# Performance work log

Hardware: AMD Instinct MI355X
Metric: run time of the kernel (lower is better)

The kernel has to match this reference:

```python
import jax, jax.numpy as jnp
import numpy as np

N_HEAD = 8
EPS = 1e-08


def setup_inputs() -> dict:
    key = jax.random.key(0)
    ks = jax.random.split(key, 4)
    B, T, C = 2, 2048, 512
    x = jax.random.normal(ks[0], (B, T, C), dtype=jnp.float32)
    attention_mask = jnp.ones((B, T, T), dtype=jnp.float32)  # causal structure irrelevant: only diagonal used
    c_attn_kernel = jax.random.normal(ks[1], (C, 3 * C), dtype=jnp.float32) * 0.02
    c_attn_bias = jnp.zeros((3 * C,), dtype=jnp.float32)
    c_proj_kernel = jax.random.normal(ks[2], (C, C), dtype=jnp.float32) * (0.02 / np.sqrt(2 * 12))
    c_proj_bias = jnp.zeros((C,), dtype=jnp.float32)
    return {
        "x": x,
        "attention_mask": attention_mask,
        "c_attn_kernel": c_attn_kernel,
        "c_attn_bias": c_attn_bias,
        "c_proj_kernel": c_proj_kernel,
        "c_proj_bias": c_proj_bias,
    }


def reference(x, attention_mask, c_attn_kernel, c_attn_bias, c_proj_kernel, c_proj_bias):
    B, T, C = x.shape
    H = N_HEAD
    D = C // H

    qkv = x @ c_attn_kernel + c_attn_bias            # (B,T,3C)
    q, k, v = jnp.split(qkv, 3, axis=2)

    # (B,T,C) -> (B,H,T,D)
    def to_heads(t):
        return t.reshape(B, T, H, D).transpose(0, 2, 1, 3)

    q, k, v = to_heads(q), to_heads(k), to_heads(v)

    phi_q = jax.nn.elu(q) + 1.0
    phi_k = jax.nn.elu(k) + 1.0

    valid_positions = jnp.diagonal(attention_mask, axis1=1, axis2=2)  # (B,T)
    position_mask = valid_positions[:, None, :, None]                 # (B,1,T,1)
    phi_k = phi_k * position_mask
    v = v * position_mask

    # (B,H,T,D,D) outer products, cumulative over time (memory-bound hot spot)
    kv_outer = jnp.einsum('bhti,bhtj->bhtij', phi_k, v)
    kv_cumsum = jnp.cumsum(kv_outer, axis=2)
    k_cumsum = jnp.cumsum(phi_k, axis=2)

    numerator = jnp.einsum('bhti,bhtij->bhtj', phi_q, kv_cumsum)      # (B,H,T,D)
    denominator = jnp.einsum('bhti,bhti->bht', phi_q, k_cumsum)       # (B,H,T)
    denominator = jnp.maximum(denominator, EPS)

    y = numerator / denominator[..., None]
    y = y.transpose(0, 2, 1, 3).reshape(B, T, C)
    y = y @ c_proj_kernel + c_proj_bias
    return y
```

## Files before the change

### kernel.cpp

```cpp
#include <hip/hip_runtime.h>
#include <math.h>

using short8 = __attribute__((ext_vector_type(8))) short;
using f32x4  = __attribute__((ext_vector_type(4))) float;
using us4    = __attribute__((ext_vector_type(4))) unsigned short;
typedef unsigned short ushort_t;

#define MFMA16(a,b,c) __builtin_amdgcn_mfma_f32_16x16x32_bf16((a),(b),(c),0,0,0)

#define BB 2
#define TT 2048
#define CC 512
#define HH 8
#define DD 64
#define N3 1536
#define NCH 32

__device__ __forceinline__ float bf2f(ushort_t u){ unsigned int x=((unsigned int)u)<<16; return __builtin_bit_cast(float,x); }
__device__ __forceinline__ ushort_t f2bf(float f){ unsigned int u=__builtin_bit_cast(unsigned int,f); u += 0x7FFFu + ((u>>16)&1u); return (ushort_t)(u>>16); }
__device__ __forceinline__ float elu1(float v){ return v > 0.f ? v + 1.f : expf(v); }

__global__ __launch_bounds__(256) void prep(const float* __restrict__ x, const float* __restrict__ amask,
                     const float* __restrict__ W, const float* __restrict__ Pw,
                     ushort_t* __restrict__ xb, ushort_t* __restrict__ wt,
                     ushort_t* __restrict__ pt, float* __restrict__ mdiag)
{
  __shared__ float tile[32][33];
  int bid = blockIdx.x, tid = threadIdx.x;
  int tx = tid & 31, ty0 = tid >> 5;
  if (bid < 768) {
    int nt = bid % 48, kt = bid / 48;
    #pragma unroll
    for (int i=0;i<4;++i){ int ty=ty0+8*i; tile[ty][tx] = W[(size_t)(kt*32+ty)*N3 + nt*32+tx]; }
    __syncthreads();
    #pragma unroll
    for (int i=0;i<4;++i){ int ty=ty0+8*i; wt[(size_t)(nt*32+ty)*CC + kt*32+tx] = f2bf(tile[tx][ty]); }
  } else if (bid < 1024) {
    int tt = bid - 768; int nt = tt & 15, kt = tt >> 4;
    #pragma unroll
    for (int i=0;i<4;++i){ int ty=ty0+8*i; tile[ty][tx] = Pw[(size_t)(kt*32+ty)*CC + nt*32+tx]; }
    __syncthreads();
    #pragma unroll
    for (int i=0;i<4;++i){ int ty=ty0+8*i; pt[(size_t)(nt*32+ty)*CC + kt*32+tx] = f2bf(tile[tx][ty]); }
  } else if (bid < 1056) {
    int g = (bid-1024)*256 + tid;
    const f32x4* xs = (const f32x4*)x;
    us4* xo = (us4*)xb;
    for (int i=g; i<(BB*TT*CC)/4; i+=32*256) {
      f32x4 v = xs[i];
      us4 o = { f2bf(v[0]), f2bf(v[1]), f2bf(v[2]), f2bf(v[3]) };
      xo[i] = o;
    }
  } else {
    for (int i=tid; i<BB*TT; i+=256) { int b=i>>11, t=i&2047; mdiag[i]=amask[((size_t)b*TT+t)*TT+t]; }
  }
}

__global__ __launch_bounds__(256) void gemm_qkv(const ushort_t* __restrict__ A, const ushort_t* __restrict__ Bt,
    const float* __restrict__ bias, const float* __restrict__ mdiag,
    ushort_t* __restrict__ phiQ, ushort_t* __restrict__ phiK,
    ushort_t* __restrict__ kTc, ushort_t* __restrict__ vTc)
{
  __shared__ __align__(16) ushort_t smem[128*72 + 64*72];
  ushort_t (*lA)[72] = (ushort_t(*)[72])smem;
  ushort_t (*lB)[72] = (ushort_t(*)[72])(smem + 128*72);
  const int tid = threadIdx.x;
  const int lane = tid & 63, wid = tid >> 6;
  const int g = lane >> 4, lr = lane & 15;
  const int bx = blockIdx.x, bm = blockIdx.y * 128;
  const int bn = bx * 64;
  const int wm = (wid >> 1) * 64, wn = (wid & 1) * 32;
  f32x4 acc[4][2] = {};

  {
    short8 nA[4], nB[2];
    #pragma unroll
    for (int it=0; it<4; ++it) { int fl = tid + it*256; nA[it] = *(const short8*)&A[(size_t)(bm + (fl>>3))*CC + (fl&7)*8]; }
    #pragma unroll
    for (int it=0; it<2; ++it) { int fl = tid + it*256; nB[it] = *(const short8*)&Bt[(size_t)(bn + (fl>>3))*CC + (fl&7)*8]; }
    #pragma unroll
    for (int it=0; it<4; ++it) { int fl = tid + it*256; *(short8*)&lA[fl>>3][(fl&7)*8] = nA[it]; }
    #pragma unroll
    for (int it=0; it<2; ++it) { int fl = tid + it*256; *(short8*)&lB[fl>>3][(fl&7)*8] = nB[it]; }
  }
  __syncthreads();

  #pragma unroll
  for (int t = 0; t < 8; ++t) {
    short8 nA[4], nB[2];
    if (t < 7) {
      int k0 = (t+1)*64;
      #pragma unroll
      for (int it=0; it<4; ++it) { int fl = tid + it*256; nA[it] = *(const short8*)&A[(size_t)(bm + (fl>>3))*CC + k0 + (fl&7)*8]; }
      #pragma unroll
      for (int it=0; it<2; ++it) { int fl = tid + it*256; nB[it] = *(const short8*)&Bt[(size_t)(bn + (fl>>3))*CC + k0 + (fl&7)*8]; }
    }
    short8 af[4][2], bf[2][2];
    #pragma unroll
    for (int mf=0; mf<4; ++mf)
      #pragma unroll
      for (int kk=0; kk<2; ++kk) af[mf][kk] = *(const short8*)&lA[wm + mf*16 + lr][kk*32 + g*8];
    #pragma unroll
    for (int nf=0; nf<2; ++nf)
      #pragma unroll
      for (int kk=0; kk<2; ++kk) bf[nf][kk] = *(const short8*)&lB[wn + nf*16 + lr][kk*32 + g*8];
    #pragma unroll
    for (int kk=0; kk<2; ++kk)
      #pragma unroll
      for (int mf=0; mf<4; ++mf)
        #pragma unroll
        for (int nf=0; nf<2; ++nf)
          acc[mf][nf] = MFMA16(af[mf][kk], bf[nf][kk], acc[mf][nf]);
    __syncthreads();
    if (t < 7) {
      #pragma unroll
      for (int it=0; it<4; ++it) { int fl = tid + it*256; *(short8*)&lA[fl>>3][(fl&7)*8] = nA[it]; }
      #pragma unroll
      for (int it=0; it<2; ++it) { int fl = tid + it*256; *(short8*)&lB[fl>>3][(fl&7)*8] = nB[it]; }
      __syncthreads();
    }
  }

  const int third = bx >> 3, h = bx & 7;
  const int b0 = bm >> 11;
  const size_t bh = (size_t)(b0*HH + h);
  ushort_t (*ldsT)[136] = (ushort_t(*)[136])smem;
  #pragma unroll
  for (int mf=0; mf<4; ++mf) {
    #pragma unroll
    for (int nf=0; nf<2; ++nf) {
      int d = wn + nf*16 + lr;
      float bs = bias[third*512 + h*64 + d];
      #pragma unroll
      for (int r=0; r<4; ++r) {
        int tl = wm + mf*16 + g*4 + r;
        int mm = bm + tl;
        int tg = mm & 2047;
        float v = acc[mf][nf][r] + bs;
        if (third == 0) {
          phiQ[(bh*TT + tg)*DD + d] = f2bf(elu1(v));
        } else if (third == 1) {
          ushort_t e = f2bf(elu1(v) * mdiag[mm]);
          phiK[(bh*TT + tg)*DD + d] = e;
          ldsT[d][tl] = e;
        } else {
          ldsT[d][tl] = f2bf(v * mdiag[mm]);
        }
      }
    }
  }
  if (third >= 1) {
    __syncthreads();
    ushort_t* dst = (third == 1) ? kTc : vTc;
    int d = tid >> 2, q = tid & 3;
    int cl = q >> 1, tl0 = (q & 1) * 32;
    int c0 = ((bm & 2047) >> 6) + cl;
    size_t obase = ((bh*NCH + c0)*DD + d)*64 + tl0;
    #pragma unroll
    for (int j=0; j<4; ++j)
      *(short8*)&dst[obase + j*8] = *(const short8*)&ldsT[d][cl*64 + tl0 + j*8];
  }
}

__global__ __launch_bounds__(256) void chunk_state(const ushort_t* __restrict__ kTc,
                                                   const ushort_t* __restrict__ vTc,
                                                   float* __restrict__ sChunk)
{
  int cid = blockIdx.x;
  int w = threadIdx.x >> 6;
  int lane = threadIdx.x & 63, g = lane >> 4, lr = lane & 15;
  size_t base = (size_t)cid * (DD*64);
  short8 af[4][2];
  #pragma unroll
  for (int mf=0; mf<4; ++mf)
    #pragma unroll
    for (int kf=0; kf<2; ++kf)
      af[mf][kf] = *(const short8*)&kTc[base + (size_t)(mf*16+lr)*64 + kf*32 + g*8];
  float* dst = &sChunk[(size_t)cid * 5120];
  short8 bfr[2];
  #pragma unroll
  for (int kf=0; kf<2; ++kf)
    bfr[kf] = *(const short8*)&vTc[base + (size_t)(w*16+lr)*64 + kf*32 + g*8];
  #pragma unroll
  for (int mf=0; mf<4; ++mf) {
    f32x4 acc = {0.f,0.f,0.f,0.f};
    #pragma unroll
    for (int kf=0; kf<2; ++kf) acc = MFMA16(af[mf][kf], bfr[kf], acc);
    *(f32x4*)&dst[(size_t)(w*16+lr)*64 + mf*16 + g*4] = acc;
  }
  if (w == 0) {
    short8 onesf;
    short ov = (lr == 0) ? (short)0x3F80 : (short)0;
    #pragma unroll
    for (int j=0;j<8;++j) onesf[j] = ov;
    #pragma unroll
    for (int mf=0; mf<4; ++mf) {
      f32x4 acc = {0.f,0.f,0.f,0.f};
      #pragma unroll
      for (int kf=0; kf<2; ++kf) acc = MFMA16(af[mf][kf], onesf, acc);
      *(f32x4*)&dst[(size_t)(64+lr)*64 + mf*16 + g*4] = acc;
    }
  }
}

__global__ __launch_bounds__(64) void scan_states(const float* __restrict__ sChunk, ushort_t* __restrict__ sPrev)
{
  int bx = blockIdx.x;
  int bh = bx / 20, seg = bx % 20;
  int e4 = seg*64 + threadIdx.x;
  const f32x4* src = (const f32x4*)(sChunk + (size_t)bh*NCH*5120) + e4;
  us4* dst = (us4*)(sPrev + (size_t)bh*NCH*5120) + e4;
  f32x4 run = {0.f,0.f,0.f,0.f};
  f32x4 p0 = src[0];
  f32x4 p1 = src[1280];
  for (int c = 0; c < NCH; ++c) {
    f32x4 cur = p0; p0 = p1;
    if (c+2 < NCH) p1 = src[(size_t)(c+2)*1280];
    us4 o = { f2bf(run[0]), f2bf(run[1]), f2bf(run[2]), f2bf(run[3]) };
    dst[(size_t)c*1280] = o;
    run += cur;
  }
}

__global__ __launch_bounds__(64) void chunk_out(const ushort_t* __restrict__ phiQ,
    const ushort_t* __restrict__ phiK, const ushort_t* __restrict__ vTc,
    const ushort_t* __restrict__ sPrev, ushort_t* __restrict__ ya)
{
  __shared__ __align__(16) ushort_t P[16][72];
  int bid = blockIdx.x;
  int q = bid & 3, cid = bid >> 2;
  int bh = cid >> 5, c = cid & 31;
  int lane = threadIdx.x, g = lane >> 4, lr = lane & 15;
  int t0 = c * 64, tq = t0 + q*16;
  size_t qbase = (size_t)bh*TT;
  size_t vbase = (size_t)cid * (DD*64);
  short8 qf[2];
  #pragma unroll
  for (int kf=0;kf<2;++kf)
    qf[kf] = *(const short8*)&phiQ[(qbase + tq + lr)*DD + kf*32 + g*8];
  f32x4 accs[4] = {};
  #pragma unroll
  for (int nf=0;nf<4;++nf)
    #pragma unroll
    for (int kf=0;kf<2;++kf) {
      short8 bk = *(const short8*)&phiK[(qbase + t0 + nf*16 + lr)*DD + kf*32 + g*8];
      accs[nf] = MFMA16(qf[kf], bk, accs[nf]);
    }
  f32x4 accn[5] = {};
  size_t sbase = (size_t)cid * 5120;
  #pragma unroll
  for (int nf=0;nf<5;++nf)
    #pragma unroll
    for (int kf=0;kf<2;++kf) {
      short8 bs = *(const short8*)&sPrev[sbase + (size_t)(nf*16+lr)*64 + kf*32 + g*8];
      accn[nf] = MFMA16(qf[kf], bs, accn[nf]);
    }
  #pragma unroll
  for (int nf=0;nf<4;++nf)
    #pragma unroll
    for (int r=0;r<4;++r) {
      int tl = g*4 + r, s = nf*16 + lr;
      P[tl][s] = f2bf((s <= q*16 + tl) ? accs[nf][r] : 0.f);
    }
  __syncthreads();
  short8 pf[2];
  #pragma unroll
  for (int kf=0;kf<2;++kf)
    pf[kf] = *(const short8*)&P[lr][kf*32 + g*8];
  short8 onesf;
  {
    short ov = (lr == 0) ? (short)0x3F80 : (short)0;
    #pragma unroll
    for (int j=0;j<8;++j) onesf[j] = ov;
  }
  #pragma unroll
  for (int nf=0;nf<5;++nf)
    #pragma unroll
    for (int kf=0;kf<2;++kf) {
      short8 vf = (nf < 4) ? *(const short8*)&vTc[vbase + (size_t)(nf*16+lr)*64 + kf*32 + g*8]
                           : onesf;
      accn[nf] = MFMA16(pf[kf], vf, accn[nf]);
    }
  float invb[4];
  #pragma unroll
  for (int r=0;r<4;++r) {
    float iv = 1.0f / fmaxf(accn[4][r], 1e-8f);
    invb[r] = __shfl(iv, lane & 48);
  }
  int b = bh >> 3, h = bh & 7;
  #pragma unroll
  for (int nf=0;nf<4;++nf)
    #pragma unroll
    for (int r=0;r<4;++r) {
      int t = tq + g*4 + r;
      int col = h*64 + nf*16 + lr;
      ya[((size_t)b*TT + t)*CC + col] = f2bf(accn[nf][r] * invb[r]);
    }
}

__global__ __launch_bounds__(256) void gemm_proj(const ushort_t* __restrict__ A, const ushort_t* __restrict__ Bt,
                                                 const float* __restrict__ bias, float* __restrict__ out)
{
  __shared__ __align__(16) ushort_t lA[32][72];
  __shared__ __align__(16) ushort_t lB[64][72];
  const int tid = threadIdx.x;
  const int lane = tid & 63, wid = tid >> 6;
  const int g = lane >> 4, lr = lane & 15;
  const int bm = blockIdx.y * 32, bn = blockIdx.x * 64;
  const int wm = (wid >> 1) * 16, wn = (wid & 1) * 32;
  f32x4 acc[2] = {};
  {
    short8 nA, nB[2];
    { int fl = tid; nA = *(const short8*)&A[(size_t)(bm + (fl>>3))*CC + (fl&7)*8]; }
    #pragma unroll
    for (int it=0; it<2; ++it) { int fl = tid + it*256; nB[it] = *(const short8*)&Bt[(size_t)(bn + (fl>>3))*CC + (fl&7)*8]; }
    { int fl = tid; *(short8*)&lA[fl>>3][(fl&7)*8] = nA; }
    #pragma unroll
    for (int it=0; it<2; ++it) { int fl = tid + it*256; *(short8*)&lB[fl>>3][(fl&7)*8] = nB[it]; }
  }
  __syncthreads();
  #pragma unroll
  for (int t = 0; t < 8; ++t) {
    short8 nA, nB[2];
    if (t < 7) {
      int k0 = (t+1)*64;
      { int fl = tid; nA = *(const short8*)&A[(size_t)(bm + (fl>>3))*CC + k0 + (fl&7)*8]; }
      #pragma unroll
      for (int it=0; it<2; ++it) { int fl = tid + it*256; nB[it] = *(const short8*)&Bt[(size_t)(bn + (fl>>3))*CC + k0 + (fl&7)*8]; }
    }
    short8 af[2], bf[2][2];
    #pragma unroll
    for (int kk=0; kk<2; ++kk) af[kk] = *(const short8*)&lA[wm + lr][kk*32 + g*8];
    #pragma unroll
    for (int nf=0; nf<2; ++nf)
      #pragma unroll
      for (int kk=0; kk<2; ++kk) bf[nf][kk] = *(const short8*)&lB[wn + nf*16 + lr][kk*32 + g*8];
    #pragma unroll
    for (int kk=0; kk<2; ++kk)
      #pragma unroll
      for (int nf=0; nf<2; ++nf)
        acc[nf] = MFMA16(af[kk], bf[nf][kk], acc[nf]);
    __syncthreads();
    if (t < 7) {
      { int fl = tid; *(short8*)&lA[fl>>3][(fl&7)*8] = nA; }
      #pragma unroll
      for (int it=0; it<2; ++it) { int fl = tid + it*256; *(short8*)&lB[fl>>3][(fl&7)*8] = nB[it]; }
      __syncthreads();
    }
  }
  int m0 = bm + wm + g*4;
  #pragma unroll
  for (int nf=0; nf<2; ++nf) {
    int n = bn + wn + nf*16 + lr;
    #pragma unroll
    for (int r=0; r<4; ++r)
      out[(size_t)(m0 + r)*CC + n] = acc[nf][r] + bias[n];
  }
}

extern "C" void kernel_launch(void* const* d_in, const int* in_sizes, int n_in,
                              void* d_out, int out_size, void* d_ws, size_t ws_size,
                              hipStream_t stream)
{
  const float* x     = (const float*)d_in[0];
  const float* amask = (const float*)d_in[1];
  const float* wqkv  = (const float*)d_in[2];
  const float* bqkv  = (const float*)d_in[3];
  const float* wproj = (const float*)d_in[4];
  const float* bproj = (const float*)d_in[5];
  float* out = (float*)d_out;
  char* ws = (char*)d_ws;

  ushort_t* xb    = (ushort_t*)(ws + 0);
  ushort_t* wt    = (ushort_t*)(ws + 4194304);
  ushort_t* pt    = (ushort_t*)(ws + 5767168);
  float*    mdiag = (float*)   (ws + 6291456);
  ushort_t* phiQ  = (ushort_t*)(ws + 6307840);
  ushort_t* phiK  = (ushort_t*)(ws + 10502144);
  ushort_t* kTc   = (ushort_t*)(ws + 14696448);
  ushort_t* vTc   = (ushort_t*)(ws + 18890752);
  ushort_t* ya    = (ushort_t*)(ws + 23085056);
  float*    sChunk= (float*)   (ws + 27279360);
  ushort_t* sPrev = (ushort_t*)(ws + 37765120);

  prep<<<dim3(1057), dim3(256), 0, stream>>>(x, amask, wqkv, wproj, xb, wt, pt, mdiag);
  gemm_qkv<<<dim3(24,32), dim3(256), 0, stream>>>(xb, wt, bqkv, mdiag, phiQ, phiK, kTc, vTc);
  chunk_state<<<dim3(512), dim3(256), 0, stream>>>(kTc, vTc, sChunk);
  scan_states<<<dim3(320), dim3(64), 0, stream>>>(sChunk, sPrev);
  chunk_out<<<dim3(2048), dim3(64), 0, stream>>>(phiQ, phiK, vTc, sPrev, ya);
  gemm_proj<<<dim3(8,128), dim3(256), 0, stream>>>(ya, pt, bproj, out);
}
```

Baseline: 171.2 us.

## Fuse input conversion into GEMMs and merge chunk state with scan

```diff
diff --git a/kernel.cpp b/kernel.cpp
--- a/kernel.cpp
+++ b/kernel.cpp
@@ -20,48 +20,13 @@
 __device__ __forceinline__ ushort_t f2bf(float f){ unsigned int u=__builtin_bit_cast(unsigned int,f); u += 0x7FFFu + ((u>>16)&1u); return (ushort_t)(u>>16); }
 __device__ __forceinline__ float elu1(float v){ return v > 0.f ? v + 1.f : expf(v); }
 
-__global__ __launch_bounds__(256) void prep(const float* __restrict__ x, const float* __restrict__ amask,
-                     const float* __restrict__ W, const float* __restrict__ Pw,
-                     ushort_t* __restrict__ xb, ushort_t* __restrict__ wt,
-                     ushort_t* __restrict__ pt, float* __restrict__ mdiag)
-{
-  __shared__ float tile[32][33];
-  int bid = blockIdx.x, tid = threadIdx.x;
-  int tx = tid & 31, ty0 = tid >> 5;
-  if (bid < 768) {
-    int nt = bid % 48, kt = bid / 48;
-    #pragma unroll
-    for (int i=0;i<4;++i){ int ty=ty0+8*i; tile[ty][tx] = W[(size_t)(kt*32+ty)*N3 + nt*32+tx]; }
-    __syncthreads();
-    #pragma unroll
-    for (int i=0;i<4;++i){ int ty=ty0+8*i; wt[(size_t)(nt*32+ty)*CC + kt*32+tx] = f2bf(tile[tx][ty]); }
-  } else if (bid < 1024) {
-    int tt = bid - 768; int nt = tt & 15, kt = tt >> 4;
-    #pragma unroll
-    for (int i=0;i<4;++i){ int ty=ty0+8*i; tile[ty][tx] = Pw[(size_t)(kt*32+ty)*CC + nt*32+tx]; }
-    __syncthreads();
-    #pragma unroll
-    for (int i=0;i<4;++i){ int ty=ty0+8*i; pt[(size_t)(nt*32+ty)*CC + kt*32+tx] = f2bf(tile[tx][ty]); }
-  } else if (bid < 1056) {
-    int g = (bid-1024)*256 + tid;
-    const f32x4* xs = (const f32x4*)x;
-    us4* xo = (us4*)xb;
-    for (int i=g; i<(BB*TT*CC)/4; i+=32*256) {
-      f32x4 v = xs[i];
-      us4 o = { f2bf(v[0]), f2bf(v[1]), f2bf(v[2]), f2bf(v[3]) };
-      xo[i] = o;
-    }
-  } else {
-    for (int i=tid; i<BB*TT; i+=256) { int b=i>>11, t=i&2047; mdiag[i]=amask[((size_t)b*TT+t)*TT+t]; }
-  }
-}
-
-__global__ __launch_bounds__(256) void gemm_qkv(const ushort_t* __restrict__ A, const ushort_t* __restrict__ Bt,
-    const float* __restrict__ bias, const float* __restrict__ mdiag,
+__global__ __launch_bounds__(256) void gemm_qkv(const float* __restrict__ X, const float* __restrict__ W,
+    const float* __restrict__ bias, const float* __restrict__ amask,
     ushort_t* __restrict__ phiQ, ushort_t* __restrict__ phiK,
     ushort_t* __restrict__ kTc, ushort_t* __restrict__ vTc)
 {
   __shared__ __align__(16) ushort_t smem[128*72 + 64*72];
+  __shared__ float ml[128];
   ushort_t (*lA)[72] = (ushort_t(*)[72])smem;
   ushort_t (*lB)[72] = (ushort_t(*)[72])(smem + 128*72);
   const int tid = threadIdx.x;
@@ -70,30 +35,52 @@
   const int bx = blockIdx.x, bm = blockIdx.y * 128;
   const int bn = bx * 64;
   const int wm = (wid >> 1) * 64, wn = (wid & 1) * 32;
+  const int b0 = bm >> 11;
+  if (tid < 128) {
+    int t = (bm + tid) & 2047;
+    ml[tid] = amask[((size_t)b0*TT + t)*TT + t];
+  }
   f32x4 acc[4][2] = {};
 
   {
-    short8 nA[4], nB[2];
-    #pragma unroll
-    for (int it=0; it<4; ++it) { int fl = tid + it*256; nA[it] = *(const short8*)&A[(size_t)(bm + (fl>>3))*CC + (fl&7)*8]; }
-    #pragma unroll
-    for (int it=0; it<2; ++it) { int fl = tid + it*256; nB[it] = *(const short8*)&Bt[(size_t)(bn + (fl>>3))*CC + (fl&7)*8]; }
-    #pragma unroll
-    for (int it=0; it<4; ++it) { int fl = tid + it*256; *(short8*)&lA[fl>>3][(fl&7)*8] = nA[it]; }
-    #pragma unroll
-    for (int it=0; it<2; ++it) { int fl = tid + it*256; *(short8*)&lB[fl>>3][(fl&7)*8] = nB[it]; }
+    #pragma unroll
+    for (int it=0; it<8; ++it) {
+      int fl = tid + it*256;
+      int row = fl >> 4, seg = fl & 15;
+      f32x4 v = *(const f32x4*)&X[(size_t)(bm+row)*CC + seg*4];
+      us4 o = { f2bf(v[0]), f2bf(v[1]), f2bf(v[2]), f2bf(v[3]) };
+      *(us4*)&lA[row][seg*4] = o;
+    }
+    #pragma unroll
+    for (int it=0; it<4; ++it) {
+      int fl = tid + it*256;
+      int krow = fl >> 4, seg = fl & 15;
+      f32x4 v = *(const f32x4*)&W[(size_t)krow*N3 + bn + seg*4];
+      lB[seg*4+0][krow] = f2bf(v[0]);
+      lB[seg*4+1][krow] = f2bf(v[1]);
+      lB[seg*4+2][krow] = f2bf(v[2]);
+      lB[seg*4+3][krow] = f2bf(v[3]);
+    }
   }
   __syncthreads();
 
   #pragma unroll
   for (int t = 0; t < 8; ++t) {
-    short8 nA[4], nB[2];
+    f32x4 nA[8], nB[4];
     if (t < 7) {
       int k0 = (t+1)*64;
       #pragma unroll
-      for (int it=0; it<4; ++it) { int fl = tid + it*256; nA[it] = *(const short8*)&A[(size_t)(bm + (fl>>3))*CC + k0 + (fl&7)*8]; }
-      #pragma unroll
-      for (int it=0; it<2; ++it) { int fl = tid + it*256; nB[it] = *(const short8*)&Bt[(size_t)(bn + (fl>>3))*CC + k0 + (fl&7)*8]; }
+      for (int it=0; it<8; ++it) {
+        int fl = tid + it*256;
+        int row = fl >> 4, seg = fl & 15;
+        nA[it] = *(const f32x4*)&X[(size_t)(bm+row)*CC + k0 + seg*4];
+      }
+      #pragma unroll
+      for (int it=0; it<4; ++it) {
+        int fl = tid + it*256;
+        int krow = fl >> 4, seg = fl & 15;
+        nB[it] = *(const f32x4*)&W[(size_t)(k0+krow)*N3 + bn + seg*4];
+      }
     }
     short8 af[4][2], bf[2][2];
     #pragma unroll
@@ -114,15 +101,26 @@
     __syncthreads();
     if (t < 7) {
       #pragma unroll
-      for (int it=0; it<4; ++it) { int fl = tid + it*256; *(short8*)&lA[fl>>3][(fl&7)*8] = nA[it]; }
-      #pragma unroll
-      for (int it=0; it<2; ++it) { int fl = tid + it*256; *(short8*)&lB[fl>>3][(fl&7)*8] = nB[it]; }
+      for (int it=0; it<8; ++it) {
+        int fl = tid + it*256;
+        int row = fl >> 4, seg = fl & 15;
+        us4 o = { f2bf(nA[it][0]), f2bf(nA[it][1]), f2bf(nA[it][2]), f2bf(nA[it][3]) };
+        *(us4*)&lA[row][seg*4] = o;
+      }
+      #pragma unroll
+      for (int it=0; it<4; ++it) {
+        int fl = tid + it*256;
+        int krow = fl >> 4, seg = fl & 15;
+        lB[seg*4+0][krow] = f2bf(nB[it][0]);
+        lB[seg*4+1][krow] = f2bf(nB[it][1]);
+        lB[seg*4+2][krow] = f2bf(nB[it][2]);
+        lB[seg*4+3][krow] = f2bf(nB[it][3]);
+      }
       __syncthreads();
     }
   }
 
   const int third = bx >> 3, h = bx & 7;
-  const int b0 = bm >> 11;
   const size_t bh = (size_t)(b0*HH + h);
   ushort_t (*ldsT)[136] = (ushort_t(*)[136])smem;
   #pragma unroll
@@ -134,17 +132,16 @@
       #pragma unroll
       for (int r=0; r<4; ++r) {
         int tl = wm + mf*16 + g*4 + r;
-        int mm = bm + tl;
-        int tg = mm & 2047;
+        int tg = (bm + tl) & 2047;
         float v = acc[mf][nf][r] + bs;
         if (third == 0) {
           phiQ[(bh*TT + tg)*DD + d] = f2bf(elu1(v));
         } else if (third == 1) {
-          ushort_t e = f2bf(elu1(v) * mdiag[mm]);
+          ushort_t e = f2bf(elu1(v) * ml[tl]);
           phiK[(bh*TT + tg)*DD + d] = e;
           ldsT[d][tl] = e;
         } else {
-          ldsT[d][tl] = f2bf(v * mdiag[mm]);
+          ldsT[d][tl] = f2bf(v * ml[tl]);
         }
       }
     }
@@ -162,63 +159,44 @@
   }
 }
 
-__global__ __launch_bounds__(256) void chunk_state(const ushort_t* __restrict__ kTc,
-                                                   const ushort_t* __restrict__ vTc,
-                                                   float* __restrict__ sChunk)
-{
-  int cid = blockIdx.x;
-  int w = threadIdx.x >> 6;
+__global__ __launch_bounds__(256) void state_scan(const ushort_t* __restrict__ kTc,
+                                                  const ushort_t* __restrict__ vTc,
+                                                  ushort_t* __restrict__ sPrev)
+{
+  int bh = blockIdx.x >> 2, jb = blockIdx.x & 3;
+  int ib = threadIdx.x >> 6;
   int lane = threadIdx.x & 63, g = lane >> 4, lr = lane & 15;
-  size_t base = (size_t)cid * (DD*64);
-  short8 af[4][2];
-  #pragma unroll
-  for (int mf=0; mf<4; ++mf)
-    #pragma unroll
-    for (int kf=0; kf<2; ++kf)
-      af[mf][kf] = *(const short8*)&kTc[base + (size_t)(mf*16+lr)*64 + kf*32 + g*8];
-  float* dst = &sChunk[(size_t)cid * 5120];
-  short8 bfr[2];
-  #pragma unroll
-  for (int kf=0; kf<2; ++kf)
-    bfr[kf] = *(const short8*)&vTc[base + (size_t)(w*16+lr)*64 + kf*32 + g*8];
-  #pragma unroll
-  for (int mf=0; mf<4; ++mf) {
-    f32x4 acc = {0.f,0.f,0.f,0.f};
-    #pragma unroll
-    for (int kf=0; kf<2; ++kf) acc = MFMA16(af[mf][kf], bfr[kf], acc);
-    *(f32x4*)&dst[(size_t)(w*16+lr)*64 + mf*16 + g*4] = acc;
-  }
-  if (w == 0) {
-    short8 onesf;
+  f32x4 acc  = {0.f,0.f,0.f,0.f};
+  f32x4 accO = {0.f,0.f,0.f,0.f};
+  short8 onesf;
+  {
     short ov = (lr == 0) ? (short)0x3F80 : (short)0;
     #pragma unroll
     for (int j=0;j<8;++j) onesf[j] = ov;
-    #pragma unroll
-    for (int mf=0; mf<4; ++mf) {
-      f32x4 acc = {0.f,0.f,0.f,0.f};
-      #pragma unroll
-      for (int kf=0; kf<2; ++kf) acc = MFMA16(af[mf][kf], onesf, acc);
-      *(f32x4*)&dst[(size_t)(64+lr)*64 + mf*16 + g*4] = acc;
-    }
-  }
-}
-
-__global__ __launch_bounds__(64) void scan_states(const float* __restrict__ sChunk, ushort_t* __restrict__ sPrev)
-{
-  int bx = blockIdx.x;
-  int bh = bx / 20, seg = bx % 20;
-  int e4 = seg*64 + threadIdx.x;
-  const f32x4* src = (const f32x4*)(sChunk + (size_t)bh*NCH*5120) + e4;
-  us4* dst = (us4*)(sPrev + (size_t)bh*NCH*5120) + e4;
-  f32x4 run = {0.f,0.f,0.f,0.f};
-  f32x4 p0 = src[0];
-  f32x4 p1 = src[1280];
+  }
   for (int c = 0; c < NCH; ++c) {
-    f32x4 cur = p0; p0 = p1;
-    if (c+2 < NCH) p1 = src[(size_t)(c+2)*1280];
-    us4 o = { f2bf(run[0]), f2bf(run[1]), f2bf(run[2]), f2bf(run[3]) };
-    dst[(size_t)c*1280] = o;
-    run += cur;
+    size_t cid = (size_t)bh*NCH + c;
+    size_t base = cid * (DD*64);
+    short8 af[2], bfr[2];
+    #pragma unroll
+    for (int kf=0; kf<2; ++kf) {
+      af[kf]  = *(const short8*)&kTc[base + (size_t)(ib*16+lr)*64 + kf*32 + g*8];
+      bfr[kf] = *(const short8*)&vTc[base + (size_t)(jb*16+lr)*64 + kf*32 + g*8];
+    }
+    {
+      us4 o = { f2bf(acc[0]), f2bf(acc[1]), f2bf(acc[2]), f2bf(acc[3]) };
+      *(us4*)&sPrev[cid*5120 + (size_t)(jb*16+lr)*64 + ib*16 + g*4] = o;
+    }
+    if (jb == 0 && lr == 0) {
+      us4 o = { f2bf(accO[0]), f2bf(accO[1]), f2bf(accO[2]), f2bf(accO[3]) };
+      *(us4*)&sPrev[cid*5120 + (size_t)64*64 + ib*16 + g*4] = o;
+    }
+    #pragma unroll
+    for (int kf=0; kf<2; ++kf) acc = MFMA16(af[kf], bfr[kf], acc);
+    if (jb == 0) {
+      #pragma unroll
+      for (int kf=0; kf<2; ++kf) accO = MFMA16(af[kf], onesf, accO);
+    }
   }
 }
 
@@ -249,12 +227,18 @@
   f32x4 accn[5] = {};
   size_t sbase = (size_t)cid * 5120;
   #pragma unroll
-  for (int nf=0;nf<5;++nf)
+  for (int nf=0;nf<4;++nf)
     #pragma unroll
     for (int kf=0;kf<2;++kf) {
       short8 bs = *(const short8*)&sPrev[sbase + (size_t)(nf*16+lr)*64 + kf*32 + g*8];
       accn[nf] = MFMA16(qf[kf], bs, accn[nf]);
     }
+  #pragma unroll
+  for (int kf=0;kf<2;++kf) {
+    short8 bs = {0,0,0,0,0,0,0,0};
+    if (lr == 0) bs = *(const short8*)&sPrev[sbase + (size_t)64*64 + kf*32 + g*8];
+    accn[4] = MFMA16(qf[kf], bs, accn[4]);
+  }
   #pragma unroll
   for (int nf=0;nf<4;++nf)
     #pragma unroll
@@ -298,7 +282,7 @@
     }
 }
 
-__global__ __launch_bounds__(256) void gemm_proj(const ushort_t* __restrict__ A, const ushort_t* __restrict__ Bt,
+__global__ __launch_bounds__(256) void gemm_proj(const ushort_t* __restrict__ A, const float* __restrict__ Pw,
                                                  const float* __restrict__ bias, float* __restrict__ out)
 {
   __shared__ __align__(16) ushort_t lA[32][72];
@@ -310,23 +294,34 @@
   const int wm = (wid >> 1) * 16, wn = (wid & 1) * 32;
   f32x4 acc[2] = {};
   {
-    short8 nA, nB[2];
-    { int fl = tid; nA = *(const short8*)&A[(size_t)(bm + (fl>>3))*CC + (fl&7)*8]; }
-    #pragma unroll
-    for (int it=0; it<2; ++it) { int fl = tid + it*256; nB[it] = *(const short8*)&Bt[(size_t)(bn + (fl>>3))*CC + (fl&7)*8]; }
-    { int fl = tid; *(short8*)&lA[fl>>3][(fl&7)*8] = nA; }
-    #pragma unroll
-    for (int it=0; it<2; ++it) { int fl = tid + it*256; *(short8*)&lB[fl>>3][(fl&7)*8] = nB[it]; }
+    int fl = tid;
+    short8 nA = *(const short8*)&A[(size_t)(bm + (fl>>3))*CC + (fl&7)*8];
+    *(short8*)&lA[fl>>3][(fl&7)*8] = nA;
+    #pragma unroll
+    for (int it=0; it<4; ++it) {
+      int f2 = tid + it*256;
+      int krow = f2 >> 4, seg = f2 & 15;
+      f32x4 v = *(const f32x4*)&Pw[(size_t)krow*CC + bn + seg*4];
+      lB[seg*4+0][krow] = f2bf(v[0]);
+      lB[seg*4+1][krow] = f2bf(v[1]);
+      lB[seg*4+2][krow] = f2bf(v[2]);
+      lB[seg*4+3][krow] = f2bf(v[3]);
+    }
   }
   __syncthreads();
   #pragma unroll
   for (int t = 0; t < 8; ++t) {
-    short8 nA, nB[2];
+    short8 nA;
+    f32x4 nB[4];
     if (t < 7) {
       int k0 = (t+1)*64;
       { int fl = tid; nA = *(const short8*)&A[(size_t)(bm + (fl>>3))*CC + k0 + (fl&7)*8]; }
       #pragma unroll
-      for (int it=0; it<2; ++it) { int fl = tid + it*256; nB[it] = *(const short8*)&Bt[(size_t)(bn + (fl>>3))*CC + k0 + (fl&7)*8]; }
+      for (int it=0; it<4; ++it) {
+        int f2 = tid + it*256;
+        int krow = f2 >> 4, seg = f2 & 15;
+        nB[it] = *(const f32x4*)&Pw[(size_t)(k0+krow)*CC + bn + seg*4];
+      }
     }
     short8 af[2], bf[2][2];
     #pragma unroll
@@ -344,7 +339,14 @@
     if (t < 7) {
       { int fl = tid; *(short8*)&lA[fl>>3][(fl&7)*8] = nA; }
       #pragma unroll
-      for (int it=0; it<2; ++it) { int fl = tid + it*256; *(short8*)&lB[fl>>3][(fl&7)*8] = nB[it]; }
+      for (int it=0; it<4; ++it) {
+        int f2 = tid + it*256;
+        int krow = f2 >> 4, seg = f2 & 15;
+        lB[seg*4+0][krow] = f2bf(nB[it][0]);
+        lB[seg*4+1][krow] = f2bf(nB[it][1]);
+        lB[seg*4+2][krow] = f2bf(nB[it][2]);
+        lB[seg*4+3][krow] = f2bf(nB[it][3]);
+      }
       __syncthreads();
     }
   }
@@ -371,22 +373,15 @@
   float* out = (float*)d_out;
   char* ws = (char*)d_ws;
 
-  ushort_t* xb    = (ushort_t*)(ws + 0);
-  ushort_t* wt    = (ushort_t*)(ws + 4194304);
-  ushort_t* pt    = (ushort_t*)(ws + 5767168);
-  float*    mdiag = (float*)   (ws + 6291456);
-  ushort_t* phiQ  = (ushort_t*)(ws + 6307840);
-  ushort_t* phiK  = (ushort_t*)(ws + 10502144);
-  ushort_t* kTc   = (ushort_t*)(ws + 14696448);
-  ushort_t* vTc   = (ushort_t*)(ws + 18890752);
-  ushort_t* ya    = (ushort_t*)(ws + 23085056);
-  float*    sChunk= (float*)   (ws + 27279360);
-  ushort_t* sPrev = (ushort_t*)(ws + 37765120);
-
-  prep<<<dim3(1057), dim3(256), 0, stream>>>(x, amask, wqkv, wproj, xb, wt, pt, mdiag);
-  gemm_qkv<<<dim3(24,32), dim3(256), 0, stream>>>(xb, wt, bqkv, mdiag, phiQ, phiK, kTc, vTc);
-  chunk_state<<<dim3(512), dim3(256), 0, stream>>>(kTc, vTc, sChunk);
-  scan_states<<<dim3(320), dim3(64), 0, stream>>>(sChunk, sPrev);
+  ushort_t* phiQ  = (ushort_t*)(ws + 0);
+  ushort_t* phiK  = (ushort_t*)(ws + 4194304);
+  ushort_t* kTc   = (ushort_t*)(ws + 8388608);
+  ushort_t* vTc   = (ushort_t*)(ws + 12582912);
+  ushort_t* ya    = (ushort_t*)(ws + 16777216);
+  ushort_t* sPrev = (ushort_t*)(ws + 20971520);
+
+  gemm_qkv<<<dim3(24,32), dim3(256), 0, stream>>>(x, wqkv, bqkv, amask, phiQ, phiK, kTc, vTc);
+  state_scan<<<dim3(64), dim3(256), 0, stream>>>(kTc, vTc, sPrev);
   chunk_out<<<dim3(2048), dim3(64), 0, stream>>>(phiQ, phiK, vTc, sPrev, ya);
-  gemm_proj<<<dim3(8,128), dim3(256), 0, stream>>>(ya, pt, bproj, out);
-}
+  gemm_proj<<<dim3(8,128), dim3(256), 0, stream>>>(ya, wproj, bproj, out);
+}
```

After: 174.6 us. 1.02x slower.
